# Kernel tuning notes

Measured on AMD Instinct MI355X. Metric: run time of the kernel, lower is better.

Reference implementation:

```python
import jax, jax.numpy as jnp
import numpy as np

N_USER, N_ITEM = 100000, 50000
E, L = 640000, 200000
F0, F1, F2 = 128, 128, 64


def _mean_agg(x_src, src, dst, n_dst):
    # gather messages from source nodes, mean-aggregate onto destination nodes
    msg = x_src[src]                                            # [E, F]
    s = jax.ops.segment_sum(msg, dst, num_segments=n_dst)       # [n_dst, F]
    cnt = jax.ops.segment_sum(jnp.ones((src.shape[0], 1), x_src.dtype), dst,
                              num_segments=n_dst)               # [n_dst, 1]
    return s / jnp.maximum(cnt, 1.0)


def _sage(x_src, x_dst, src, dst, n_dst, Wl, b, Wr):
    # PyG SAGEConv: lin_l(mean_aggr(x_src)) + lin_r(x_dst)
    agg = _mean_agg(x_src, src, dst, n_dst)
    return agg @ Wl + b + x_dst @ Wr


def setup_inputs() -> dict:
    key = jax.random.key(0)
    ks = jax.random.split(key, 20)
    inp = {}
    inp['x_user'] = jax.random.normal(ks[0], (N_USER, F0), jnp.float32)
    inp['x_item'] = jax.random.normal(ks[1], (N_ITEM, F0), jnp.float32)
    inp['src_u'] = jax.random.randint(ks[2], (E,), 0, N_USER)
    inp['dst_i'] = jax.random.randint(ks[3], (E,), 0, N_ITEM)
    inp['el_src'] = jax.random.randint(ks[4], (L,), 0, N_USER)
    inp['el_dst'] = jax.random.randint(ks[5], (L,), 0, N_ITEM)
    # SAGEConv params per edge type per layer: Wl (neighbor), bias, Wr (root)
    def w(k, fi, fo):
        return jax.random.normal(k, (fi, fo), jnp.float32) * (1.0 / np.sqrt(fi))
    inp['Wl_ui1'] = w(ks[6], F0, F1);  inp['b_ui1'] = jnp.zeros((F1,), jnp.float32)
    inp['Wr_ui1'] = w(ks[7], F0, F1)
    inp['Wl_iu1'] = w(ks[8], F0, F1);  inp['b_iu1'] = jnp.zeros((F1,), jnp.float32)
    inp['Wr_iu1'] = w(ks[9], F0, F1)
    inp['Wl_ui2'] = w(ks[10], F1, F2); inp['b_ui2'] = jnp.zeros((F2,), jnp.float32)
    inp['Wr_ui2'] = w(ks[11], F1, F2)
    inp['Wl_iu2'] = w(ks[12], F1, F2); inp['b_iu2'] = jnp.zeros((F2,), jnp.float32)
    inp['Wr_iu2'] = w(ks[13], F1, F2)
    return inp


def reference(x_user, x_item, src_u, dst_i, el_src, el_dst,
              Wl_ui1, b_ui1, Wr_ui1, Wl_iu1, b_iu1, Wr_iu1,
              Wl_ui2, b_ui2, Wr_ui2, Wl_iu2, b_iu2, Wr_iu2):
    # layer 1 (to_hetero: one SAGEConv per edge type; relu per node type; eval -> no dropout)
    h_i1 = jax.nn.relu(_sage(x_user, x_item, src_u, dst_i, N_ITEM, Wl_ui1, b_ui1, Wr_ui1))
    h_u1 = jax.nn.relu(_sage(x_item, x_user, dst_i, src_u, N_USER, Wl_iu1, b_iu1, Wr_iu1))
    # layer 2
    h_i2 = _sage(h_u1, h_i1, src_u, dst_i, N_ITEM, Wl_ui2, b_ui2, Wr_ui2)
    h_u2 = _sage(h_i1, h_u1, dst_i, src_u, N_USER, Wl_iu2, b_iu2, Wr_iu2)
    # LPsimple_classif: gather endpoints, elementwise product, sum over features
    pred = (h_u2[el_src] * h_i2[el_dst]).sum(axis=-1)           # [L]
    return pred
```

## Files before the change

kernel.cpp:

```cpp
#include <hip/hip_runtime.h>

#define NUSER 100000
#define NITEM 50000
#define NEDGE 640000
#define NLINK 200000
#define GI 49
#define GU 98
#define NBU1 782
#define NBI1 391
#define NBG1 (NBU1 + NBI1)
#define FCHUNK 4096
#define FNCH 157

typedef unsigned int  uint;
typedef unsigned short ushort_t;
typedef __attribute__((ext_vector_type(8))) short bf16x8;
typedef __attribute__((ext_vector_type(4))) float f32x4;
typedef __attribute__((ext_vector_type(4))) uint  u32x4;

__device__ __forceinline__ ushort_t f2bf(float f) {
    uint u = __float_as_uint(f);
    u += 0x7FFFu + ((u >> 16) & 1u);
    return (ushort_t)(u >> 16);
}
__device__ __forceinline__ float bf2f(ushort_t h) { return __uint_as_float(((uint)h) << 16); }
__device__ __forceinline__ float lo16f(uint u) { return __uint_as_float(u << 16); }
__device__ __forceinline__ float hi16f(uint u) { return __uint_as_float(u & 0xFFFF0000u); }

__global__ __launch_bounds__(256) void countw_kernel(
    const int* __restrict__ src, const int* __restrict__ dst,
    int* __restrict__ cnt_u, int* __restrict__ cnt_i,
    const float* __restrict__ Wl0, const float* __restrict__ Wr0,
    const float* __restrict__ Wl1, const float* __restrict__ Wr1,
    const float* __restrict__ Wl2, const float* __restrict__ Wr2,
    const float* __restrict__ Wl3, const float* __restrict__ Wr3,
    ushort_t* __restrict__ Bh0, ushort_t* __restrict__ Bl0,
    ushort_t* __restrict__ Bh1, ushort_t* __restrict__ Bl1,
    ushort_t* __restrict__ Bh2, ushort_t* __restrict__ Bl2,
    ushort_t* __restrict__ Bh3, ushort_t* __restrict__ Bl3)
{
    if (blockIdx.x < 2500) {
        int e = blockIdx.x * 256 + threadIdx.x;
        if (e >= NEDGE) return;
        atomicAdd(&cnt_u[src[e]], 1);
        atomicAdd(&cnt_i[dst[e]], 1);
        return;
    }
    int b = blockIdx.x - 2500;
    const float *Wl, *Wr; ushort_t *Bh, *Bl; int FO, t;
    if (b < 16)      { Wl = Wl0; Wr = Wr0; Bh = Bh0; Bl = Bl0; FO = 128; t = b * 256 + threadIdx.x; }
    else if (b < 32) { Wl = Wl1; Wr = Wr1; Bh = Bh1; Bl = Bl1; FO = 128; t = (b - 16) * 256 + threadIdx.x; }
    else if (b < 40) { Wl = Wl2; Wr = Wr2; Bh = Bh2; Bl = Bl2; FO = 64;  t = (b - 32) * 256 + threadIdx.x; }
    else             { Wl = Wl3; Wr = Wr3; Bh = Bh3; Bl = Bl3; FO = 64;  t = (b - 40) * 256 + threadIdx.x; }
    int lane = t & 63, ks = (t >> 6) & 3, nt = t >> 8;
    int col = nt * 16 + (lane & 15);
    int k0 = ks * 32 + (lane >> 4) * 8;
    const float* W = (col < FO) ? Wl : Wr;
    int cc = (col < FO) ? col : col - FO;
#pragma unroll
    for (int j = 0; j < 8; ++j) {
        float v = W[(size_t)(k0 + j) * FO + cc];
        ushort_t h = f2bf(v);
        Bh[(size_t)t * 8 + j] = h;
        Bl[(size_t)t * 8 + j] = f2bf(v - bf2f(h));
    }
}

__global__ __launch_bounds__(256) void scan1_kernel(
    const int* __restrict__ cnt_i, const int* __restrict__ cnt_u,
    int* __restrict__ head_i, int* __restrict__ head_u,
    int* __restrict__ bsum_i, int* __restrict__ bsum_u)
{
    __shared__ int sh[256];
    int b = blockIdx.x, t = threadIdx.x;
    const int* cnt; int* head; int* bsum; int n, cb;
    if (b < GI) { cnt = cnt_i; head = head_i; bsum = bsum_i; n = NITEM; cb = b; }
    else        { cnt = cnt_u; head = head_u; bsum = bsum_u; n = NUSER; cb = b - GI; }
    int base = cb * 1024 + t * 4;
    int4 v = {0, 0, 0, 0};
    if (base + 3 < n) v = *(const int4*)(cnt + base);
    else {
        if (base + 0 < n) v.x = cnt[base + 0];
        if (base + 1 < n) v.y = cnt[base + 1];
        if (base + 2 < n) v.z = cnt[base + 2];
    }
    int s = v.x + v.y + v.z + v.w;
    sh[t] = s;
    __syncthreads();
    for (int o = 1; o < 256; o <<= 1) {
        int a = (t >= o) ? sh[t - o] : 0;
        __syncthreads();
        sh[t] += a;
        __syncthreads();
    }
    int excl = sh[t] - s;
    if (t == 255) bsum[cb] = sh[255];
    if (base + 0 < n) head[base + 0] = excl;
    if (base + 1 < n) head[base + 1] = excl + v.x;
    if (base + 2 < n) head[base + 2] = excl + v.x + v.y;
    if (base + 3 < n) head[base + 3] = excl + v.x + v.y + v.z;
}

__global__ __launch_bounds__(256) void scan23_kernel(
    int* __restrict__ head_i, int* __restrict__ head_u,
    const int* __restrict__ bsum_i, const int* __restrict__ bsum_u)
{
    __shared__ int sh[256];
    int b = blockIdx.x, t = threadIdx.x;
    int* head; const int* bsum; int n, cb;
    if (b < GI) { head = head_i; bsum = bsum_i; n = NITEM; cb = b; }
    else        { head = head_u; bsum = bsum_u; n = NUSER; cb = b - GI; }
    sh[t] = (t < cb) ? bsum[t] : 0;
    __syncthreads();
    for (int o = 128; o >= 1; o >>= 1) {
        if (t < o) sh[t] += sh[t + o];
        __syncthreads();
    }
    int add = sh[0];
    int base = cb * 1024 + t * 4;
#pragma unroll
    for (int k = 0; k < 4; ++k)
        if (base + k < n) head[base + k] += add;
}

template <int NO, bool ASPLIT>
__device__ __forceinline__ void gemm_body(
    const void* __restrict__ A_,
    const ushort_t* __restrict__ Bh, const ushort_t* __restrict__ Bl,
    ushort_t* __restrict__ ymsg, ushort_t* __restrict__ zout,
    int n, int row0, u32x4 (*ashH)[16], u32x4 (*ashL)[16])
{
    constexpr int CT = NO / 128;
    constexpr int FO = NO / 2;
    const int tid = threadIdx.x;
    const int lane = tid & 63, wv = tid >> 6;
    const int lr = lane & 15, lg = lane >> 4;
    const int row = tid >> 4, ch = tid & 15;

    bf16x8 bfh[4][CT], bfl[4][CT];
#pragma unroll
    for (int ks = 0; ks < 4; ++ks)
#pragma unroll
        for (int ct = 0; ct < CT; ++ct) {
            size_t boff = ((size_t)((wv * CT + ct) * 4 + ks) * 64 + lane) * 8;
            bfh[ks][ct] = __builtin_bit_cast(bf16x8, *(const u32x4*)(Bh + boff));
            bfl[ks][ct] = __builtin_bit_cast(bf16x8, *(const u32x4*)(Bl + boff));
        }

    f32x4 c0 = {0.f, 0.f, 0.f, 0.f}, c1 = {0.f, 0.f, 0.f, 0.f};
    u32x4 cq = {0u, 0u, 0u, 0u};
    {
        int grow = row0 + row;
        if (grow < n) {
            if (ASPLIT) {
                const f32x4* p = (const f32x4*)((const float*)A_ + (size_t)grow * 128 + ch * 8);
                c0 = p[0]; c1 = p[1];
            } else {
                cq = *(const u32x4*)((const ushort_t*)A_ + (size_t)grow * 128 + ch * 8);
            }
        }
    }

#pragma unroll
    for (int st = 0; st < 4; ++st) {
        int sc = ch ^ (row & 7);
        if (ASPLIT) {
            float e[8];
#pragma unroll
            for (int j = 0; j < 4; ++j) { e[j] = c0[j]; e[4 + j] = c1[j]; }
            uint hv[4], lv[4];
#pragma unroll
            for (int j = 0; j < 4; ++j) {
                ushort_t h0 = f2bf(e[2 * j]), h1 = f2bf(e[2 * j + 1]);
                hv[j] = (uint)h0 | ((uint)h1 << 16);
                ushort_t l0 = f2bf(e[2 * j] - bf2f(h0)), l1 = f2bf(e[2 * j + 1] - bf2f(h1));
                lv[j] = (uint)l0 | ((uint)l1 << 16);
            }
            u32x4 hq = {hv[0], hv[1], hv[2], hv[3]};
            u32x4 lq = {lv[0], lv[1], lv[2], lv[3]};
            ashH[row][sc] = hq;
            ashL[row][sc] = lq;
        } else {
            ashH[row][sc] = cq;
        }
        __syncthreads();

        if (st < 3) {
            c0 = f32x4{0.f, 0.f, 0.f, 0.f}; c1 = f32x4{0.f, 0.f, 0.f, 0.f};
            cq = u32x4{0u, 0u, 0u, 0u};
            int grow = row0 + (st + 1) * 32 + row;
            if (grow < n) {
                if (ASPLIT) {
                    const f32x4* p = (const f32x4*)((const float*)A_ + (size_t)grow * 128 + ch * 8);
                    c0 = p[0]; c1 = p[1];
                } else {
                    cq = *(const u32x4*)((const ushort_t*)A_ + (size_t)grow * 128 + ch * 8);
                }
            }
        }

        f32x4 acc[2][CT];
#pragma unroll
        for (int rt = 0; rt < 2; ++rt)
#pragma unroll
            for (int ct = 0; ct < CT; ++ct) { f32x4 zz = {0.f, 0.f, 0.f, 0.f}; acc[rt][ct] = zz; }
#pragma unroll
        for (int ks = 0; ks < 4; ++ks) {
            bf16x8 ah[2], al[2];
#pragma unroll
            for (int rt = 0; rt < 2; ++rt) {
                int arow = rt * 16 + lr;
                int pos = (ks * 4 + lg) ^ (arow & 7);
                ah[rt] = __builtin_bit_cast(bf16x8, ashH[arow][pos]);
                if (ASPLIT) al[rt] = __builtin_bit_cast(bf16x8, ashL[arow][pos]);
            }
#pragma unroll
            for (int ct = 0; ct < CT; ++ct)
#pragma unroll
                for (int rt = 0; rt < 2; ++rt) {
                    acc[rt][ct] = __builtin_amdgcn_mfma_f32_16x16x32_bf16(ah[rt], bfh[ks][ct], acc[rt][ct], 0, 0, 0);
                    acc[rt][ct] = __builtin_amdgcn_mfma_f32_16x16x32_bf16(ah[rt], bfl[ks][ct], acc[rt][ct], 0, 0, 0);
                    if (ASPLIT)
                        acc[rt][ct] = __builtin_amdgcn_mfma_f32_16x16x32_bf16(al[rt], bfh[ks][ct], acc[rt][ct], 0, 0, 0);
                }
        }

#pragma unroll
        for (int rt = 0; rt < 2; ++rt)
#pragma unroll
            for (int ct = 0; ct < CT; ++ct) {
                int col = wv * (NO / 8) + ct * 16 + lr;
                bool ism = col < FO;
                ushort_t* dstp = ism ? ymsg : zout;
                int cc = ism ? col : col - FO;
#pragma unroll
                for (int r = 0; r < 4; ++r) {
                    int orow = row0 + st * 32 + rt * 16 + lg * 4 + r;
                    if (orow < n) dstp[(size_t)orow * FO + cc] = f2bf(acc[rt][ct][r]);
                }
            }
        __syncthreads();
    }
}

__global__ __launch_bounds__(512) void gemmfill_kernel(
    const float* __restrict__ xu, const float* __restrict__ xi,
    const ushort_t* __restrict__ Bh0, const ushort_t* __restrict__ Bl0,
    const ushort_t* __restrict__ Bh1, const ushort_t* __restrict__ Bl1,
    ushort_t* __restrict__ y0, ushort_t* __restrict__ z0,
    ushort_t* __restrict__ y1, ushort_t* __restrict__ z1,
    const int* __restrict__ src, const int* __restrict__ dst,
    int* __restrict__ head_i, int* __restrict__ head_u,
    int* __restrict__ nbr_i, int* __restrict__ nbr_u)
{
    if (blockIdx.x >= NBG1) {
        int b = blockIdx.x - NBG1;
        int pass = b / (2 * FNCH);
        int rem  = b % (2 * FNCH);
        int dir  = rem / FNCH;
        int base = (rem % FNCH) * FCHUNK;
        int e_end = min(base + FCHUNK, NEDGE);
        if (dir == 0) {
            int lo = pass * (NITEM / 8), hi = lo + NITEM / 8;
            for (int e = base + threadIdx.x; e < e_end; e += 512) {
                int d = dst[e];
                if (d >= lo && d < hi) nbr_i[atomicAdd(&head_i[d], 1)] = src[e];
            }
        } else {
            int lo = pass * (NUSER / 8), hi = lo + NUSER / 8;
            for (int e = base + threadIdx.x; e < e_end; e += 512) {
                int s = src[e];
                if (s >= lo && s < hi) nbr_u[atomicAdd(&head_u[s], 1)] = dst[e];
            }
        }
        return;
    }
    __shared__ u32x4 ashH[32][16];
    __shared__ u32x4 ashL[32][16];
    if ((int)blockIdx.x < NBU1)
        gemm_body<256, true>(xu, Bh0, Bl0, y0, z0, NUSER, blockIdx.x * 128, ashH, ashL);
    else
        gemm_body<256, true>(xi, Bh1, Bl1, y1, z1, NITEM, (blockIdx.x - NBU1) * 128, ashH, ashL);
}

__global__ __launch_bounds__(512) void gemm2_kernel(
    const ushort_t* __restrict__ A0, const ushort_t* __restrict__ A1,
    const ushort_t* __restrict__ Bh0, const ushort_t* __restrict__ Bl0,
    const ushort_t* __restrict__ Bh1, const ushort_t* __restrict__ Bl1,
    ushort_t* __restrict__ y0, ushort_t* __restrict__ z0,
    ushort_t* __restrict__ y1, ushort_t* __restrict__ z1)
{
    __shared__ u32x4 ashH[32][16];
    if ((int)blockIdx.x < NBU1)
        gemm_body<128, false>(A0, Bh0, Bl0, y0, z0, NUSER, blockIdx.x * 128, ashH, ashH);
    else
        gemm_body<128, false>(A1, Bh1, Bl1, y1, z1, NITEM, (blockIdx.x - NBU1) * 128, ashH, ashH);
}

__global__ __launch_bounds__(256) void gather1_kernel(
    const ushort_t* __restrict__ ymsg_u, const ushort_t* __restrict__ ymsg_i,
    const int* __restrict__ nbr_i, const int* __restrict__ head_i, const int* __restrict__ cnt_i,
    const int* __restrict__ nbr_u, const int* __restrict__ head_u, const int* __restrict__ cnt_u,
    const ushort_t* __restrict__ z_i, const ushort_t* __restrict__ z_u,
    const float* __restrict__ b_ui, const float* __restrict__ b_iu,
    ushort_t* __restrict__ h1_i, ushort_t* __restrict__ h1_u)
{
    int w = (blockIdx.x << 2) + (threadIdx.x >> 6);
    const ushort_t *ym, *z; const int *nbr, *head, *cnt; const float* bias;
    ushort_t* hout; int node;
    if (w < NITEM) { ym = ymsg_u; nbr = nbr_i; head = head_i; cnt = cnt_i; z = z_i; bias = b_ui; hout = h1_i; node = w; }
    else if (w < NITEM + NUSER) { ym = ymsg_i; nbr = nbr_u; head = head_u; cnt = cnt_u; z = z_u; bias = b_iu; hout = h1_u; node = w - NITEM; }
    else return;
    int lane = threadIdx.x & 63;
    int c = cnt[node], end = head[node];
    int j = end - c;
    const uint* Y = (const uint*)ym;
    float ax = 0.f, ay = 0.f;
    for (; j + 7 < end; j += 8) {
        uint u0 = Y[(size_t)nbr[j + 0] * 64 + lane];
        uint u1 = Y[(size_t)nbr[j + 1] * 64 + lane];
        uint u2 = Y[(size_t)nbr[j + 2] * 64 + lane];
        uint u3 = Y[(size_t)nbr[j + 3] * 64 + lane];
        uint u4 = Y[(size_t)nbr[j + 4] * 64 + lane];
        uint u5 = Y[(size_t)nbr[j + 5] * 64 + lane];
        uint u6 = Y[(size_t)nbr[j + 6] * 64 + lane];
        uint u7 = Y[(size_t)nbr[j + 7] * 64 + lane];
        ax += lo16f(u0) + lo16f(u1) + lo16f(u2) + lo16f(u3)
            + lo16f(u4) + lo16f(u5) + lo16f(u6) + lo16f(u7);
        ay += hi16f(u0) + hi16f(u1) + hi16f(u2) + hi16f(u3)
            + hi16f(u4) + hi16f(u5) + hi16f(u6) + hi16f(u7);
    }
    for (; j + 1 < end; j += 2) {
        uint u0 = Y[(size_t)nbr[j + 0] * 64 + lane];
        uint u1 = Y[(size_t)nbr[j + 1] * 64 + lane];
        ax += lo16f(u0) + lo16f(u1);
        ay += hi16f(u0) + hi16f(u1);
    }
    if (j < end) {
        uint u0 = Y[(size_t)nbr[j] * 64 + lane];
        ax += lo16f(u0); ay += hi16f(u0);
    }
    float m = 1.f / fmaxf((float)c, 1.f);
    uint zu = ((const uint*)z)[(size_t)node * 64 + lane];
    float vx = fmaxf(ax * m + lo16f(zu) + bias[lane * 2], 0.f);
    float vy = fmaxf(ay * m + hi16f(zu) + bias[lane * 2 + 1], 0.f);
    ((uint*)hout)[(size_t)node * 64 + lane] = (uint)f2bf(vx) | ((uint)f2bf(vy) << 16);
}

__global__ __launch_bounds__(256) void gather2_kernel(
    const ushort_t* __restrict__ ymsg_u, const ushort_t* __restrict__ ymsg_i,
    const int* __restrict__ nbr_i, const int* __restrict__ head_i, const int* __restrict__ cnt_i,
    const int* __restrict__ nbr_u, const int* __restrict__ head_u, const int* __restrict__ cnt_u,
    const ushort_t* __restrict__ z_i, const ushort_t* __restrict__ z_u,
    const float* __restrict__ b_ui, const float* __restrict__ b_iu,
    ushort_t* __restrict__ h2_i, ushort_t* __restrict__ h2_u)
{
    int w = (blockIdx.x << 2) + (threadIdx.x >> 6);
    const ushort_t *ym, *z; const int *nbr, *head, *cnt; const float* bias;
    ushort_t* hout; int node;
    if (w < NITEM) { ym = ymsg_u; nbr = nbr_i; head = head_i; cnt = cnt_i; z = z_i; bias = b_ui; hout = h2_i; node = w; }
    else if (w < NITEM + NUSER) { ym = ymsg_i; nbr = nbr_u; head = head_u; cnt = cnt_u; z = z_u; bias = b_iu; hout = h2_u; node = w - NITEM; }
    else return;
    int lane = threadIdx.x & 63;
    int c = cnt[node], end = head[node];
    int j = end - c;
    float a = 0.f;
    for (; j + 7 < end; j += 8) {
        a += bf2f(ym[(size_t)nbr[j + 0] * 64 + lane]) + bf2f(ym[(size_t)nbr[j + 1] * 64 + lane])
           + bf2f(ym[(size_t)nbr[j + 2] * 64 + lane]) + bf2f(ym[(size_t)nbr[j + 3] * 64 + lane])
           + bf2f(ym[(size_t)nbr[j + 4] * 64 + lane]) + bf2f(ym[(size_t)nbr[j + 5] * 64 + lane])
           + bf2f(ym[(size_t)nbr[j + 6] * 64 + lane]) + bf2f(ym[(size_t)nbr[j + 7] * 64 + lane]);
    }
    for (; j + 1 < end; j += 2)
        a += bf2f(ym[(size_t)nbr[j] * 64 + lane]) + bf2f(ym[(size_t)nbr[j + 1] * 64 + lane]);
    if (j < end) a += bf2f(ym[(size_t)nbr[j] * 64 + lane]);
    float m = 1.f / fmaxf((float)c, 1.f);
    float v = a * m + bf2f(z[(size_t)node * 64 + lane]) + bias[lane];
    hout[(size_t)node * 64 + lane] = f2bf(v);
}

__global__ __launch_bounds__(256) void predict_kernel(
    const int* __restrict__ el_src, const int* __restrict__ el_dst,
    const ushort_t* __restrict__ hu, const ushort_t* __restrict__ hi,
    float* __restrict__ out)
{
    int l = (blockIdx.x << 2) + (threadIdx.x >> 6);
    if (l >= NLINK) return;
    int lane = threadIdx.x & 63;
    int u = el_src[l];
    int it = el_dst[l];
    float v = bf2f(hu[(size_t)u * 64 + lane]) * bf2f(hi[(size_t)it * 64 + lane]);
#pragma unroll
    for (int o = 32; o >= 1; o >>= 1) v += __shfl_down(v, o, 64);
    if (lane == 0) out[l] = v;
}

extern "C" void kernel_launch(void* const* d_in, const int* in_sizes, int n_in,
                              void* d_out, int out_size, void* d_ws, size_t ws_size,
                              hipStream_t stream) {
    const float* x_user = (const float*)d_in[0];
    const float* x_item = (const float*)d_in[1];
    const int*   src_u  = (const int*)d_in[2];
    const int*   dst_i  = (const int*)d_in[3];
    const int*   el_src = (const int*)d_in[4];
    const int*   el_dst = (const int*)d_in[5];
    const float* Wl_ui1 = (const float*)d_in[6];
    const float* b_ui1  = (const float*)d_in[7];
    const float* Wr_ui1 = (const float*)d_in[8];
    const float* Wl_iu1 = (const float*)d_in[9];
    const float* b_iu1  = (const float*)d_in[10];
    const float* Wr_iu1 = (const float*)d_in[11];
    const float* Wl_ui2 = (const float*)d_in[12];
    const float* b_ui2  = (const float*)d_in[13];
    const float* Wr_ui2 = (const float*)d_in[14];
    const float* Wl_iu2 = (const float*)d_in[15];
    const float* b_iu2  = (const float*)d_in[16];
    const float* Wr_iu2 = (const float*)d_in[17];
    float* out = (float*)d_out;

    int* iw     = (int*)d_ws;
    int* cnt_i  = iw;
    int* cnt_u  = iw + 50000;
    int* bsum_i = iw + 150000;
    int* bsum_u = iw + 150064;
    int* head_i = iw + 150192;
    int* head_u = iw + 200192;
    int* nbr_i  = iw + 300192;
    int* nbr_u  = iw + 940192;
    char* W8 = (char*)d_ws;
    size_t off = 6320768;
    ushort_t* Bh1u = (ushort_t*)(W8 + off); off += 65536;
    ushort_t* Bl1u = (ushort_t*)(W8 + off); off += 65536;
    ushort_t* Bh1i = (ushort_t*)(W8 + off); off += 65536;
    ushort_t* Bl1i = (ushort_t*)(W8 + off); off += 65536;
    ushort_t* Bh2u = (ushort_t*)(W8 + off); off += 32768;
    ushort_t* Bl2u = (ushort_t*)(W8 + off); off += 32768;
    ushort_t* Bh2i = (ushort_t*)(W8 + off); off += 32768;
    ushort_t* Bl2i = (ushort_t*)(W8 + off); off += 32768;
    ushort_t* h1_u = (ushort_t*)(W8 + off); off += (size_t)NUSER * 128 * 2;
    ushort_t* h1_i = (ushort_t*)(W8 + off); off += (size_t)NITEM * 128 * 2;
    size_t YB = off;
    ushort_t* ymsg_u = (ushort_t*)(W8 + YB);
    ushort_t* ymsg_i = (ushort_t*)(W8 + YB + 25600000);
    ushort_t* z_u    = (ushort_t*)(W8 + YB + 38400000);
    ushort_t* z_i    = (ushort_t*)(W8 + YB + 64000000);
    ushort_t* ymsg2_u = (ushort_t*)(W8 + YB);
    ushort_t* ymsg2_i = (ushort_t*)(W8 + YB + 12800000);
    ushort_t* z2_u    = (ushort_t*)(W8 + YB + 19200000);
    ushort_t* z2_i    = (ushort_t*)(W8 + YB + 32000000);
    ushort_t* h2_u    = (ushort_t*)(W8 + YB + 38400000);
    ushort_t* h2_i    = (ushort_t*)(W8 + YB + 51200000);

    hipMemsetAsync(d_ws, 0, 150000 * sizeof(int), stream);

    countw_kernel<<<2548, 256, 0, stream>>>(
        src_u, dst_i, cnt_u, cnt_i,
        Wl_ui1, Wr_iu1, Wl_iu1, Wr_ui1, Wl_ui2, Wr_iu2, Wl_iu2, Wr_ui2,
        Bh1u, Bl1u, Bh1i, Bl1i, Bh2u, Bl2u, Bh2i, Bl2i);

    scan1_kernel<<<GI + GU, 256, 0, stream>>>(cnt_i, cnt_u, head_i, head_u, bsum_i, bsum_u);
    scan23_kernel<<<GI + GU, 256, 0, stream>>>(head_i, head_u, bsum_i, bsum_u);

    gemmfill_kernel<<<NBG1 + 8 * 2 * FNCH, 512, 0, stream>>>(
        x_user, x_item, Bh1u, Bl1u, Bh1i, Bl1i,
        ymsg_u, z_u, ymsg_i, z_i,
        src_u, dst_i, head_i, head_u, nbr_i, nbr_u);

    gather1_kernel<<<(NITEM + NUSER) / 4, 256, 0, stream>>>(
        ymsg_u, ymsg_i, nbr_i, head_i, cnt_i, nbr_u, head_u, cnt_u,
        z_i, z_u, b_ui1, b_iu1, h1_i, h1_u);

    gemm2_kernel<<<NBG1, 512, 0, stream>>>(
        h1_u, h1_i, Bh2u, Bl2u, Bh2i, Bl2i,
        ymsg2_u, z2_u, ymsg2_i, z2_i);
    gather2_kernel<<<(NITEM + NUSER) / 4, 256, 0, stream>>>(
        ymsg2_u, ymsg2_i, nbr_i, head_i, cnt_i, nbr_u, head_u, cnt_u,
        z2_i, z2_u, b_ui2, b_iu2, h2_i, h2_u);

    predict_kernel<<<NLINK / 4, 256, 0, stream>>>(el_src, el_dst, h2_u, h2_i, out);
}
```

Baseline: 363.6 us.

## Restructure GEMM tiles: B in LDS, A direct to registers, split output columns

The GEMM body now stages the weight fragments for one output half (message or root projection) in shared memory and loads A rows straight from global memory into MFMA operand registers, with the next k-slice prefetched. Each block covers 256 rows and one column group, so the grid doubles and there are no per-stage barriers or A staging through LDS. This cuts register pressure from holding all B fragments and removes the A-tile LDS round trip. In exchange, each A row is read twice, once per column group, and the A loads are less coalesced (16-byte per-lane row reads).

```diff
diff --git a/kernel.cpp b/kernel.cpp
--- a/kernel.cpp
+++ b/kernel.cpp
@@ -6,9 +6,9 @@
 #define NLINK 200000
 #define GI 49
 #define GU 98
-#define NBU1 782
-#define NBI1 391
-#define NBG1 (NBU1 + NBI1)
+#define NBU 391
+#define NBI 196
+#define NBGEMM (2 * (NBU + NBI))
 #define FCHUNK 4096
 #define FNCH 157
 
@@ -123,124 +123,112 @@
         if (base + k < n) head[base + k] += add;
 }
 
-template <int NO, bool ASPLIT>
+template <int FO, bool ASPLIT>
 __device__ __forceinline__ void gemm_body(
     const void* __restrict__ A_,
     const ushort_t* __restrict__ Bh, const ushort_t* __restrict__ Bl,
-    ushort_t* __restrict__ ymsg, ushort_t* __restrict__ zout,
-    int n, int row0, u32x4 (*ashH)[16], u32x4 (*ashL)[16])
-{
-    constexpr int CT = NO / 128;
-    constexpr int FO = NO / 2;
-    const int tid = threadIdx.x;
-    const int lane = tid & 63, wv = tid >> 6;
+    ushort_t* __restrict__ dstp, int n, int row0, int cg,
+    u32x4* __restrict__ bshH, u32x4* __restrict__ bshL)
+{
+    constexpr int CT = FO / 16;
+    constexpr int NB = CT * 4 * 64;
+    const u32x4* gh = (const u32x4*)Bh + (size_t)cg * NB;
+    const u32x4* gl = (const u32x4*)Bl + (size_t)cg * NB;
+    for (int idx = threadIdx.x; idx < NB; idx += 512) {
+        bshH[idx] = gh[idx];
+        bshL[idx] = gl[idx];
+    }
+    __syncthreads();
+
+    const int lane = threadIdx.x & 63, wv = threadIdx.x >> 6;
     const int lr = lane & 15, lg = lane >> 4;
-    const int row = tid >> 4, ch = tid & 15;
-
-    bf16x8 bfh[4][CT], bfl[4][CT];
-#pragma unroll
-    for (int ks = 0; ks < 4; ++ks)
-#pragma unroll
-        for (int ct = 0; ct < CT; ++ct) {
-            size_t boff = ((size_t)((wv * CT + ct) * 4 + ks) * 64 + lane) * 8;
-            bfh[ks][ct] = __builtin_bit_cast(bf16x8, *(const u32x4*)(Bh + boff));
-            bfl[ks][ct] = __builtin_bit_cast(bf16x8, *(const u32x4*)(Bl + boff));
-        }
-
-    f32x4 c0 = {0.f, 0.f, 0.f, 0.f}, c1 = {0.f, 0.f, 0.f, 0.f};
-    u32x4 cq = {0u, 0u, 0u, 0u};
-    {
-        int grow = row0 + row;
-        if (grow < n) {
+    const int wrow0 = row0 + wv * 32;
+    const int r0 = wrow0 + lr, r1 = wrow0 + 16 + lr;
+
+    f32x4 acc[2][CT];
+#pragma unroll
+    for (int rt = 0; rt < 2; ++rt)
+#pragma unroll
+        for (int ct = 0; ct < CT; ++ct) { f32x4 zz = {0.f, 0.f, 0.f, 0.f}; acc[rt][ct] = zz; }
+
+    f32x4 f0c[2], f1c[2]; u32x4 qc[2];
+#define LOAD_A(KS)                                                              \
+    {                                                                           \
+        int kb = (KS) * 32 + lg * 8;                                            \
+        int rows[2] = {r0, r1};                                                 \
+        _Pragma("unroll")                                                       \
+        for (int rt = 0; rt < 2; ++rt) {                                        \
+            if (ASPLIT) {                                                       \
+                f0c[rt] = f32x4{0.f, 0.f, 0.f, 0.f};                            \
+                f1c[rt] = f32x4{0.f, 0.f, 0.f, 0.f};                            \
+                if (rows[rt] < n) {                                             \
+                    const f32x4* p = (const f32x4*)((const float*)A_ +          \
+                        (size_t)rows[rt] * 128 + kb);                           \
+                    f0c[rt] = p[0]; f1c[rt] = p[1];                             \
+                }                                                               \
+            } else {                                                            \
+                qc[rt] = u32x4{0u, 0u, 0u, 0u};                                 \
+                if (rows[rt] < n)                                               \
+                    qc[rt] = *(const u32x4*)((const ushort_t*)A_ +              \
+                        (size_t)rows[rt] * 128 + kb);                           \
+            }                                                                   \
+        }                                                                       \
+    }
+
+    LOAD_A(0);
+#pragma unroll
+    for (int ks = 0; ks < 4; ++ks) {
+        bf16x8 ah[2], al[2];
+#pragma unroll
+        for (int rt = 0; rt < 2; ++rt) {
             if (ASPLIT) {
-                const f32x4* p = (const f32x4*)((const float*)A_ + (size_t)grow * 128 + ch * 8);
-                c0 = p[0]; c1 = p[1];
+                float e[8];
+#pragma unroll
+                for (int j = 0; j < 4; ++j) { e[j] = f0c[rt][j]; e[4 + j] = f1c[rt][j]; }
+                uint hv[4], lv[4];
+#pragma unroll
+                for (int j = 0; j < 4; ++j) {
+                    ushort_t h0 = f2bf(e[2 * j]), h1 = f2bf(e[2 * j + 1]);
+                    hv[j] = (uint)h0 | ((uint)h1 << 16);
+                    ushort_t l0 = f2bf(e[2 * j] - bf2f(h0)), l1 = f2bf(e[2 * j + 1] - bf2f(h1));
+                    lv[j] = (uint)l0 | ((uint)l1 << 16);
+                }
+                u32x4 hq = {hv[0], hv[1], hv[2], hv[3]};
+                u32x4 lq = {lv[0], lv[1], lv[2], lv[3]};
+                ah[rt] = __builtin_bit_cast(bf16x8, hq);
+                al[rt] = __builtin_bit_cast(bf16x8, lq);
             } else {
-                cq = *(const u32x4*)((const ushort_t*)A_ + (size_t)grow * 128 + ch * 8);
+                ah[rt] = __builtin_bit_cast(bf16x8, qc[rt]);
             }
         }
-    }
-
-#pragma unroll
-    for (int st = 0; st < 4; ++st) {
-        int sc = ch ^ (row & 7);
-        if (ASPLIT) {
-            float e[8];
-#pragma unroll
-            for (int j = 0; j < 4; ++j) { e[j] = c0[j]; e[4 + j] = c1[j]; }
-            uint hv[4], lv[4];
-#pragma unroll
-            for (int j = 0; j < 4; ++j) {
-                ushort_t h0 = f2bf(e[2 * j]), h1 = f2bf(e[2 * j + 1]);
-                hv[j] = (uint)h0 | ((uint)h1 << 16);
-                ushort_t l0 = f2bf(e[2 * j] - bf2f(h0)), l1 = f2bf(e[2 * j + 1] - bf2f(h1));
-                lv[j] = (uint)l0 | ((uint)l1 << 16);
-            }
-            u32x4 hq = {hv[0], hv[1], hv[2], hv[3]};
-            u32x4 lq = {lv[0], lv[1], lv[2], lv[3]};
-            ashH[row][sc] = hq;
-            ashL[row][sc] = lq;
-        } else {
-            ashH[row][sc] = cq;
-        }
-        __syncthreads();
-
-        if (st < 3) {
-            c0 = f32x4{0.f, 0.f, 0.f, 0.f}; c1 = f32x4{0.f, 0.f, 0.f, 0.f};
-            cq = u32x4{0u, 0u, 0u, 0u};
-            int grow = row0 + (st + 1) * 32 + row;
-            if (grow < n) {
-                if (ASPLIT) {
-                    const f32x4* p = (const f32x4*)((const float*)A_ + (size_t)grow * 128 + ch * 8);
-                    c0 = p[0]; c1 = p[1];
-                } else {
-                    cq = *(const u32x4*)((const ushort_t*)A_ + (size_t)grow * 128 + ch * 8);
-                }
+        if (ks < 3) LOAD_A(ks + 1);
+
+#pragma unroll
+        for (int ct = 0; ct < CT; ++ct) {
+            bf16x8 bh = __builtin_bit_cast(bf16x8, bshH[(ct * 4 + ks) * 64 + lane]);
+            bf16x8 bl = __builtin_bit_cast(bf16x8, bshL[(ct * 4 + ks) * 64 + lane]);
+#pragma unroll
+            for (int rt = 0; rt < 2; ++rt) {
+                acc[rt][ct] = __builtin_amdgcn_mfma_f32_16x16x32_bf16(ah[rt], bh, acc[rt][ct], 0, 0, 0);
+                acc[rt][ct] = __builtin_amdgcn_mfma_f32_16x16x32_bf16(ah[rt], bl, acc[rt][ct], 0, 0, 0);
+                if (ASPLIT)
+                    acc[rt][ct] = __builtin_amdgcn_mfma_f32_16x16x32_bf16(al[rt], bh, acc[rt][ct], 0, 0, 0);
             }
         }
-
-        f32x4 acc[2][CT];
-#pragma unroll
-        for (int rt = 0; rt < 2; ++rt)
-#pragma unroll
-            for (int ct = 0; ct < CT; ++ct) { f32x4 zz = {0.f, 0.f, 0.f, 0.f}; acc[rt][ct] = zz; }
-#pragma unroll
-        for (int ks = 0; ks < 4; ++ks) {
-            bf16x8 ah[2], al[2];
-#pragma unroll
-            for (int rt = 0; rt < 2; ++rt) {
-                int arow = rt * 16 + lr;
-                int pos = (ks * 4 + lg) ^ (arow & 7);
-                ah[rt] = __builtin_bit_cast(bf16x8, ashH[arow][pos]);
-                if (ASPLIT) al[rt] = __builtin_bit_cast(bf16x8, ashL[arow][pos]);
+    }
+#undef LOAD_A
+
+#pragma unroll
+    for (int rt = 0; rt < 2; ++rt)
+#pragma unroll
+        for (int ct = 0; ct < CT; ++ct) {
+            int cc = ct * 16 + lr;
+#pragma unroll
+            for (int r = 0; r < 4; ++r) {
+                int orow = wrow0 + rt * 16 + lg * 4 + r;
+                if (orow < n) dstp[(size_t)orow * FO + cc] = f2bf(acc[rt][ct][r]);
             }
-#pragma unroll
-            for (int ct = 0; ct < CT; ++ct)
-#pragma unroll
-                for (int rt = 0; rt < 2; ++rt) {
-                    acc[rt][ct] = __builtin_amdgcn_mfma_f32_16x16x32_bf16(ah[rt], bfh[ks][ct], acc[rt][ct], 0, 0, 0);
-                    acc[rt][ct] = __builtin_amdgcn_mfma_f32_16x16x32_bf16(ah[rt], bfl[ks][ct], acc[rt][ct], 0, 0, 0);
-                    if (ASPLIT)
-                        acc[rt][ct] = __builtin_amdgcn_mfma_f32_16x16x32_bf16(al[rt], bfh[ks][ct], acc[rt][ct], 0, 0, 0);
-                }
         }
-
-#pragma unroll
-        for (int rt = 0; rt < 2; ++rt)
-#pragma unroll
-            for (int ct = 0; ct < CT; ++ct) {
-                int col = wv * (NO / 8) + ct * 16 + lr;
-                bool ism = col < FO;
-                ushort_t* dstp = ism ? ymsg : zout;
-                int cc = ism ? col : col - FO;
-#pragma unroll
-                for (int r = 0; r < 4; ++r) {
-                    int orow = row0 + st * 32 + rt * 16 + lg * 4 + r;
-                    if (orow < n) dstp[(size_t)orow * FO + cc] = f2bf(acc[rt][ct][r]);
-                }
-            }
-        __syncthreads();
-    }
 }
 
 __global__ __launch_bounds__(512) void gemmfill_kernel(
@@ -253,8 +241,8 @@
     int* __restrict__ head_i, int* __restrict__ head_u,
     int* __restrict__ nbr_i, int* __restrict__ nbr_u)
 {
-    if (blockIdx.x >= NBG1) {
-        int b = blockIdx.x - NBG1;
+    if (blockIdx.x >= NBGEMM) {
+        int b = blockIdx.x - NBGEMM;
         int pass = b / (2 * FNCH);
         int rem  = b % (2 * FNCH);
         int dir  = rem / FNCH;
@@ -275,12 +263,17 @@
         }
         return;
     }
-    __shared__ u32x4 ashH[32][16];
-    __shared__ u32x4 ashL[32][16];
-    if ((int)blockIdx.x < NBU1)
-        gemm_body<256, true>(xu, Bh0, Bl0, y0, z0, NUSER, blockIdx.x * 128, ashH, ashL);
-    else
-        gemm_body<256, true>(xi, Bh1, Bl1, y1, z1, NITEM, (blockIdx.x - NBU1) * 128, ashH, ashL);
+    __shared__ u32x4 bshH[2048];
+    __shared__ u32x4 bshL[2048];
+    int bid = blockIdx.x;
+    if (bid < 2 * NBU) {
+        int rowblk = bid >> 1, cg = bid & 1;
+        gemm_body<128, true>(xu, Bh0, Bl0, cg == 0 ? y0 : z0, NUSER, rowblk * 256, cg, bshH, bshL);
+    } else {
+        int b2 = bid - 2 * NBU;
+        int rowblk = b2 >> 1, cg = b2 & 1;
+        gemm_body<128, true>(xi, Bh1, Bl1, cg == 0 ? y1 : z1, NITEM, rowblk * 256, cg, bshH, bshL);
+    }
 }
 
 __global__ __launch_bounds__(512) void gemm2_kernel(
@@ -290,11 +283,17 @@
     ushort_t* __restrict__ y0, ushort_t* __restrict__ z0,
     ushort_t* __restrict__ y1, ushort_t* __restrict__ z1)
 {
-    __shared__ u32x4 ashH[32][16];
-    if ((int)blockIdx.x < NBU1)
-        gemm_body<128, false>(A0, Bh0, Bl0, y0, z0, NUSER, blockIdx.x * 128, ashH, ashH);
-    else
-        gemm_body<128, false>(A1, Bh1, Bl1, y1, z1, NITEM, (blockIdx.x - NBU1) * 128, ashH, ashH);
+    __shared__ u32x4 bshH[1024];
+    __shared__ u32x4 bshL[1024];
+    int bid = blockIdx.x;
+    if (bid < 2 * NBU) {
+        int rowblk = bid >> 1, cg = bid & 1;
+        gemm_body<64, false>(A0, Bh0, Bl0, cg == 0 ? y0 : z0, NUSER, rowblk * 256, cg, bshH, bshL);
+    } else {
+        int b2 = bid - 2 * NBU;
+        int rowblk = b2 >> 1, cg = b2 & 1;
+        gemm_body<64, false>(A1, Bh1, Bl1, cg == 0 ? y1 : z1, NITEM, rowblk * 256, cg, bshH, bshL);
+    }
 }
 
 __global__ __launch_bounds__(256) void gather1_kernel(
@@ -461,7 +460,7 @@
     scan1_kernel<<<GI + GU, 256, 0, stream>>>(cnt_i, cnt_u, head_i, head_u, bsum_i, bsum_u);
     scan23_kernel<<<GI + GU, 256, 0, stream>>>(head_i, head_u, bsum_i, bsum_u);
 
-    gemmfill_kernel<<<NBG1 + 8 * 2 * FNCH, 512, 0, stream>>>(
+    gemmfill_kernel<<<NBGEMM + 8 * 2 * FNCH, 512, 0, stream>>>(
         x_user, x_item, Bh1u, Bl1u, Bh1i, Bl1i,
         ymsg_u, z_u, ymsg_i, z_i,
         src_u, dst_i, head_i, head_u, nbr_i, nbr_u);
@@ -470,7 +469,7 @@
         ymsg_u, ymsg_i, nbr_i, head_i, cnt_i, nbr_u, head_u, cnt_u,
         z_i, z_u, b_ui1, b_iu1, h1_i, h1_u);
 
-    gemm2_kernel<<<NBG1, 512, 0, stream>>>(
+    gemm2_kernel<<<NBGEMM, 512, 0, stream>>>(
         h1_u, h1_i, Bh2u, Bl2u, Bh2i, Bl2i,
         ymsg2_u, z2_u, ymsg2_i, z2_i);
     gather2_kernel<<<(NITEM + NUSER) / 4, 256, 0, stream>>>(
```

Result: slower. 371.8 us (+2.3%).
